# Optimization experiments

Measured on AMD Instinct MI355X. Metric: run time of the kernel, lower is better.

Reference implementation:

```python
import jax, jax.numpy as jnp
import numpy as np

N_LINKS = 7
BATCH = 524288
# alternating joint axes (z,y,z,y,z,y,z), Panda-like serial chain
AXES = np.array([[0,0,1],[0,1,0],[0,0,1],[0,1,0],[0,0,1],[0,1,0],[0,0,1]], dtype=np.float32)


def _skew(a):
    # a: [3] -> [3,3]
    return jnp.array([[0.0, -a[2], a[1]], [a[2], 0.0, -a[0]], [-a[1], a[0], 0.0]], dtype=a.dtype)


def _rot_to_quat(R):
    # R: [..., 3, 3] -> quaternion [..., 4] in (x, y, z, w) order
    r00, r11, r22 = R[..., 0, 0], R[..., 1, 1], R[..., 2, 2]
    eps = 1e-9
    qw = 0.5 * jnp.sqrt(jnp.clip(1.0 + r00 + r11 + r22, eps))
    qx = 0.5 * jnp.sqrt(jnp.clip(1.0 + r00 - r11 - r22, eps))
    qy = 0.5 * jnp.sqrt(jnp.clip(1.0 - r00 + r11 - r22, eps))
    qz = 0.5 * jnp.sqrt(jnp.clip(1.0 - r00 - r11 + r22, eps))
    sx = jnp.where(R[..., 2, 1] - R[..., 1, 2] < 0, -1.0, 1.0)
    sy = jnp.where(R[..., 0, 2] - R[..., 2, 0] < 0, -1.0, 1.0)
    sz = jnp.where(R[..., 1, 0] - R[..., 0, 1] < 0, -1.0, 1.0)
    return jnp.stack([sx * qx, sy * qy, sz * qz, qw], axis=-1)


def setup_inputs() -> dict:
    key = jax.random.key(0)
    k1, k2, k3 = jax.random.split(key, 3)
    q = jax.random.normal(k1, (BATCH, N_LINKS), dtype=jnp.float32)
    raw = jax.random.normal(k2, (N_LINKS, 3, 3), dtype=jnp.float32)
    Q, _ = jnp.linalg.qr(raw)
    det = jnp.linalg.det(Q)
    rot_fixed = Q * det[:, None, None]  # proper rotations, det=+1
    trans_fixed = 0.2 * jax.random.normal(k3, (N_LINKS, 3), dtype=jnp.float32)
    return {"q": q, "rot_fixed": rot_fixed, "trans_fixed": trans_fixed}


def _fk(q, rot_fixed, trans_fixed):
    # q: [B, N], rot_fixed: [N,3,3], trans_fixed: [N,3]
    B = q.shape[0]
    axes = jnp.asarray(AXES)
    skews = jnp.stack([_skew(axes[i]) for i in range(N_LINKS)])  # [N,3,3]
    outers = jnp.einsum('ni,nj->nij', axes, axes)  # [N,3,3]
    I3 = jnp.eye(3, dtype=q.dtype)

    def step(carry, xs):
        Rp, tp = carry  # parent pose: [B,3,3], [B,3]
        Rf, tf, K, A, qi = xs  # [3,3],[3],[3,3],[3,3],[B]
        c = jnp.cos(qi)[:, None, None]
        s = jnp.sin(qi)[:, None, None]
        Raxis = c * I3 + s * K + (1.0 - c) * A  # Rodrigues, [B,3,3]
        Rj = jnp.einsum('ij,bjk->bik', Rf, Raxis)  # joint pose rotation
        R = jnp.einsum('bij,bjk->bik', Rp, Rj)  # world rotation
        t = jnp.einsum('bij,j->bi', Rp, tf) + tp  # world translation
        return (R, t), (R, t)

    R0 = jnp.broadcast_to(I3, (B, 3, 3))
    t0 = jnp.zeros((B, 3), dtype=q.dtype)
    xs = (rot_fixed, trans_fixed, skews, outers, q.T)
    _, (Rs, ts) = jax.lax.scan(step, (R0, t0), xs)
    # Rs: [N,B,3,3], ts: [N,B,3]
    quats = _rot_to_quat(Rs)  # [N,B,4]
    return ts, quats


def reference(q, rot_fixed, trans_fixed):
    return _fk(q, rot_fixed, trans_fixed)
```

## Files before the change

kernel.cpp:

```cpp
#include <hip/hip_runtime.h>

#define NL 7

__global__ __launch_bounds__(256) void fk_kernel(
    const float* __restrict__ q,
    const float* __restrict__ rotf,
    const float* __restrict__ trf,
    float* __restrict__ out,
    int B)
{
    __shared__ float sR[NL * 9];
    __shared__ float st[NL * 3];
    __shared__ float sQ[256 * NL];
    __shared__ float sT[NL * 256 * 3];

    const int tid = threadIdx.x;
    const int blockBase = blockIdx.x * 256;

    if (tid < NL * 9) sR[tid] = rotf[tid];
    if (tid >= 64 && tid < 64 + NL * 3) st[tid - 64] = trf[tid - 64];

    const size_t qbase = (size_t)blockBase * NL;
#pragma unroll
    for (int k = 0; k < NL; k++)
        sQ[k * 256 + tid] = q[qbase + (size_t)k * 256 + tid];
    __syncthreads();

    float qv[NL];
#pragma unroll
    for (int i = 0; i < NL; i++) qv[i] = sQ[tid * NL + i];

    const int b = blockBase + tid;

    float R00 = 1.f, R01 = 0.f, R02 = 0.f;
    float R10 = 0.f, R11 = 1.f, R12 = 0.f;
    float R20 = 0.f, R21 = 0.f, R22 = 1.f;
    float t0 = 0.f, t1 = 0.f, t2 = 0.f;

    const size_t QOFF = (size_t)NL * B * 3;

#pragma unroll
    for (int i = 0; i < NL; i++) {
        float s, c;
        __sincosf(qv[i], &s, &c);

        const float f0 = st[i * 3 + 0], f1 = st[i * 3 + 1], f2 = st[i * 3 + 2];
        t0 += R00 * f0 + R01 * f1 + R02 * f2;
        t1 += R10 * f0 + R11 * f1 + R12 * f2;
        t2 += R20 * f0 + R21 * f1 + R22 * f2;

        const float F00 = sR[i * 9 + 0], F01 = sR[i * 9 + 1], F02 = sR[i * 9 + 2];
        const float F10 = sR[i * 9 + 3], F11 = sR[i * 9 + 4], F12 = sR[i * 9 + 5];
        const float F20 = sR[i * 9 + 6], F21 = sR[i * 9 + 7], F22 = sR[i * 9 + 8];
        const float M00 = R00 * F00 + R01 * F10 + R02 * F20;
        const float M01 = R00 * F01 + R01 * F11 + R02 * F21;
        const float M02 = R00 * F02 + R01 * F12 + R02 * F22;
        const float M10 = R10 * F00 + R11 * F10 + R12 * F20;
        const float M11 = R10 * F01 + R11 * F11 + R12 * F21;
        const float M12 = R10 * F02 + R11 * F12 + R12 * F22;
        const float M20 = R20 * F00 + R21 * F10 + R22 * F20;
        const float M21 = R20 * F01 + R21 * F11 + R22 * F21;
        const float M22 = R20 * F02 + R21 * F12 + R22 * F22;

        if ((i & 1) == 0) {
            R00 = M00 * c + M01 * s;  R01 = M01 * c - M00 * s;  R02 = M02;
            R10 = M10 * c + M11 * s;  R11 = M11 * c - M10 * s;  R12 = M12;
            R20 = M20 * c + M21 * s;  R21 = M21 * c - M20 * s;  R22 = M22;
        } else {
            R00 = M00 * c - M02 * s;  R01 = M01;  R02 = M00 * s + M02 * c;
            R10 = M10 * c - M12 * s;  R11 = M11;  R12 = M10 * s + M12 * c;
            R20 = M20 * c - M22 * s;  R21 = M21;  R22 = M20 * s + M22 * c;
        }

        const float eps = 1e-9f;
        float qw = 0.5f * sqrtf(fmaxf(1.f + R00 + R11 + R22, eps));
        float qx = 0.5f * sqrtf(fmaxf(1.f + R00 - R11 - R22, eps));
        float qy = 0.5f * sqrtf(fmaxf(1.f - R00 + R11 - R22, eps));
        float qz = 0.5f * sqrtf(fmaxf(1.f - R00 - R11 + R22, eps));
        qx = (R21 - R12 < 0.f) ? -qx : qx;
        qy = (R02 - R20 < 0.f) ? -qy : qy;
        qz = (R10 - R01 < 0.f) ? -qz : qz;

        sT[i * 768 + tid * 3 + 0] = t0;
        sT[i * 768 + tid * 3 + 1] = t1;
        sT[i * 768 + tid * 3 + 2] = t2;

        float4 pq;
        pq.x = qx; pq.y = qy; pq.z = qz; pq.w = qw;
        *reinterpret_cast<float4*>(out + QOFF + ((size_t)i * B + b) * 4) = pq;
    }

    __syncthreads();

#pragma unroll
    for (int i = 0; i < NL; i++) {
        const size_t obase = ((size_t)i * B + blockBase) * 3;
#pragma unroll
        for (int k = 0; k < 3; k++)
            out[obase + k * 256 + tid] = sT[i * 768 + k * 256 + tid];
    }
}

extern "C" void kernel_launch(void* const* d_in, const int* in_sizes, int n_in,
                              void* d_out, int out_size, void* d_ws, size_t ws_size,
                              hipStream_t stream) {
    const float* q    = (const float*)d_in[0];
    const float* rotf = (const float*)d_in[1];
    const float* trf  = (const float*)d_in[2];
    float* out = (float*)d_out;

    int B;
    if (out_size > 0 && out_size % 49 == 0) B = out_size / 49;
    else                                    B = in_sizes[0] / NL;

    const int grid = B / 256;
    fk_kernel<<<grid, 256, 0, stream>>>(q, rotf, trf, out, B);
}
```

Before: 119.9 us.

## Double-buffer translation staging in LDS and use nontemporal stores

Shrinks the shared translation buffer from all seven links to a two-slot ping-pong buffer, so each link's translations are written out inside the loop after a per-link barrier. This cuts LDS use per block so more blocks can be resident (launch bounds now request 8). It also switches the output stores to nontemporal, reads joint angles straight from LDS instead of registers, and uses the raw hardware sqrt builtin. The cost is seven block-wide barriers per block instead of one.

```diff
diff --git a/kernel.cpp b/kernel.cpp
--- a/kernel.cpp
+++ b/kernel.cpp
@@ -2,7 +2,9 @@
 
 #define NL 7
 
-__global__ __launch_bounds__(256) void fk_kernel(
+typedef float vfloat4 __attribute__((ext_vector_type(4)));
+
+__global__ __launch_bounds__(256, 8) void fk_kernel(
     const float* __restrict__ q,
     const float* __restrict__ rotf,
     const float* __restrict__ trf,
@@ -12,7 +14,7 @@
     __shared__ float sR[NL * 9];
     __shared__ float st[NL * 3];
     __shared__ float sQ[256 * NL];
-    __shared__ float sT[NL * 256 * 3];
+    __shared__ float sT[2][768];
 
     const int tid = threadIdx.x;
     const int blockBase = blockIdx.x * 256;
@@ -26,10 +28,6 @@
         sQ[k * 256 + tid] = q[qbase + (size_t)k * 256 + tid];
     __syncthreads();
 
-    float qv[NL];
-#pragma unroll
-    for (int i = 0; i < NL; i++) qv[i] = sQ[tid * NL + i];
-
     const int b = blockBase + tid;
 
     float R00 = 1.f, R01 = 0.f, R02 = 0.f;
@@ -42,7 +40,7 @@
 #pragma unroll
     for (int i = 0; i < NL; i++) {
         float s, c;
-        __sincosf(qv[i], &s, &c);
+        __sincosf(sQ[tid * NL + i], &s, &c);
 
         const float f0 = st[i * 3 + 0], f1 = st[i * 3 + 1], f2 = st[i * 3 + 2];
         t0 += R00 * f0 + R01 * f1 + R02 * f2;
@@ -73,31 +71,29 @@
         }
 
         const float eps = 1e-9f;
-        float qw = 0.5f * sqrtf(fmaxf(1.f + R00 + R11 + R22, eps));
-        float qx = 0.5f * sqrtf(fmaxf(1.f + R00 - R11 - R22, eps));
-        float qy = 0.5f * sqrtf(fmaxf(1.f - R00 + R11 - R22, eps));
-        float qz = 0.5f * sqrtf(fmaxf(1.f - R00 - R11 + R22, eps));
+        float qw = 0.5f * __builtin_amdgcn_sqrtf(fmaxf(1.f + R00 + R11 + R22, eps));
+        float qx = 0.5f * __builtin_amdgcn_sqrtf(fmaxf(1.f + R00 - R11 - R22, eps));
+        float qy = 0.5f * __builtin_amdgcn_sqrtf(fmaxf(1.f - R00 + R11 - R22, eps));
+        float qz = 0.5f * __builtin_amdgcn_sqrtf(fmaxf(1.f - R00 - R11 + R22, eps));
         qx = (R21 - R12 < 0.f) ? -qx : qx;
         qy = (R02 - R20 < 0.f) ? -qy : qy;
         qz = (R10 - R01 < 0.f) ? -qz : qz;
 
-        sT[i * 768 + tid * 3 + 0] = t0;
-        sT[i * 768 + tid * 3 + 1] = t1;
-        sT[i * 768 + tid * 3 + 2] = t2;
+        vfloat4 pq;
+        pq.x = qx; pq.y = qy; pq.z = qz; pq.w = qw;
+        __builtin_nontemporal_store(
+            pq, reinterpret_cast<vfloat4*>(out + QOFF + ((size_t)i * B + b) * 4));
 
-        float4 pq;
-        pq.x = qx; pq.y = qy; pq.z = qz; pq.w = qw;
-        *reinterpret_cast<float4*>(out + QOFF + ((size_t)i * B + b) * 4) = pq;
-    }
+        float* tb = sT[i & 1];
+        tb[tid * 3 + 0] = t0;
+        tb[tid * 3 + 1] = t1;
+        tb[tid * 3 + 2] = t2;
+        __syncthreads();
 
-    __syncthreads();
-
-#pragma unroll
-    for (int i = 0; i < NL; i++) {
         const size_t obase = ((size_t)i * B + blockBase) * 3;
 #pragma unroll
         for (int k = 0; k < 3; k++)
-            out[obase + k * 256 + tid] = sT[i * 768 + k * 256 + tid];
+            __builtin_nontemporal_store(tb[k * 256 + tid], out + obase + k * 256 + tid);
     }
 }
 
```

New measurement: 125.8 us. 5.0% more time.
